# Optimization experiments

Hardware: AMD Instinct MI355X
Metric: run time of the kernel (lower is better)

The kernel has to match this reference:

```python
import jax, jax.numpy as jnp
import numpy as np

VOCAB = 32000
D = 256
NB = 32          # n_bubbles
NEQ = 5          # n_equilibrium_steps
SEQ = 64


def setup_inputs() -> dict:
    key = jax.random.key(0)
    k1, k2, k3 = jax.random.split(key, 3)
    tokens = jax.random.randint(k1, (SEQ,), 0, VOCAB)
    E = jax.random.normal(k2, (VOCAB, D), dtype=jnp.float32) * 0.02
    bubbles = jax.random.normal(k3, (NB, D), dtype=jnp.float32) * 0.02
    return {
        "tokens": tokens,
        "E": E,
        "bubbles": bubbles,
        "memory_decay_base": jnp.float32(0.8),
        "novelty_sensitivity": jnp.float32(1.0),
    }


def _foam(bubbles, x):
    """Foam equilibrium stand-in.
    bubbles: [NB, D] learned bubble states; x: [D] input.
    Returns (equilibrium [NB,D], rho [D,D], output_dist [NB]).
    rho is a trace-1 density matrix over normalized bubble states.
    """
    scale = 1.0 / np.sqrt(D)
    s = bubbles
    for _ in range(NEQ):  # fixed small count of equilibrium steps
        w = jax.nn.softmax(s @ x * scale)            # [NB]
        s = s + w[:, None] * (x[None, :] - s)        # relax toward input
    p = jax.nn.softmax(s @ x * scale)                # output_dist [NB]
    sn = s / (jnp.linalg.norm(s, axis=-1, keepdims=True) + 1e-10)
    rho = jnp.einsum('b,bi,bj->ij', p, sn, sn)       # [D, D], trace == 1
    return s, rho, p


def reference(tokens, E, bubbles, memory_decay_base, novelty_sensitivity):
    sens = jnp.abs(novelty_sensitivity)

    def step(memory, tok):
        x = E[tok]                                   # [D]
        mm = memory.mean(axis=0)                     # [D]
        mem_norm = jnp.linalg.norm(mm) + 1e-10
        x_norm = jnp.linalg.norm(x) + 1e-10
        novelty = jnp.where(mem_norm > 1e-8,
                            1.0 - jnp.dot(x, mm) / (x_norm * mem_norm),
                            jnp.float32(1.0))
        decay = jax.nn.sigmoid(memory_decay_base - sens * novelty)
        x_wm = x + decay * mm
        eq, rho, p = _foam(bubbles, x_wm)
        memory = decay * memory + (1.0 - decay) * eq
        # Born rule: logit_v = e_v^T rho e_v   -> [VOCAB]
        logits = ((E @ rho) * E).sum(axis=-1)
        return memory, logits

    mem0 = jnp.zeros((NB, D), jnp.float32)
    _, logits = jax.lax.scan(step, mem0, tokens)
    return logits  # [SEQ, VOCAB]
```

## Files before the change

kernel.cpp:

```cpp
#include <hip/hip_runtime.h>
#include <math.h>

#define VOCAB 32000
#define D 256
#define NB 32
#define NEQ 5
#define SEQ 64
#define NBASIS 96

#define WS_S     0
#define WS_COEF  (NBASIS*NBASIS)
#define WS_U     (WS_COEF + SEQ*NBASIS)
#define WS_VV    (WS_U + SEQ*NB)
#define WS_C     (WS_VV + SEQ*NB)
#define WS_WHL   (WS_C + SEQ)

typedef __attribute__((ext_vector_type(8))) short short8v;
typedef __attribute__((ext_vector_type(4))) float f32x4;

__global__ __launch_bounds__(256) void foam_grams(
    const int* __restrict__ tokens, const float* __restrict__ E,
    const float* __restrict__ bubbles, float* __restrict__ ws)
{
    const int idx = blockIdx.x * 256 + threadIdx.x;
    const int i = idx / NBASIS, j = idx % NBASIS;
    const float4* ra = (const float4*)((i < NB) ? (bubbles + i * D)
                                                : (E + (long)tokens[i - NB] * D));
    const float4* rb = (const float4*)((j < NB) ? (bubbles + j * D)
                                                : (E + (long)tokens[j - NB] * D));
    float a0 = 0.f, a1 = 0.f, a2 = 0.f, a3 = 0.f;
    #pragma unroll
    for (int k = 0; k < D / 4; k += 4) {
        float4 x, y;
        x = ra[k];     y = rb[k];
        a0 = fmaf(x.x, y.x, fmaf(x.y, y.y, fmaf(x.z, y.z, fmaf(x.w, y.w, a0))));
        x = ra[k + 1]; y = rb[k + 1];
        a1 = fmaf(x.x, y.x, fmaf(x.y, y.y, fmaf(x.z, y.z, fmaf(x.w, y.w, a1))));
        x = ra[k + 2]; y = rb[k + 2];
        a2 = fmaf(x.x, y.x, fmaf(x.y, y.y, fmaf(x.z, y.z, fmaf(x.w, y.w, a2))));
        x = ra[k + 3]; y = rb[k + 3];
        a3 = fmaf(x.x, y.x, fmaf(x.y, y.y, fmaf(x.z, y.z, fmaf(x.w, y.w, a3))));
    }
    ws[WS_S + i * NBASIS + j] = (a0 + a1) + (a2 + a3);
}

template <int CTRL>
__device__ __forceinline__ float dpp_add(float x) {
    int yi = __builtin_amdgcn_update_dpp(0, __float_as_int(x), CTRL, 0xF, 0xF, true);
    return x + __int_as_float(yi);
}
__device__ __forceinline__ float xor16_add(float x) {
    float a, b;
    asm("v_mov_b32 %0, %2\n\t"
        "v_mov_b32 %1, %2\n\t"
        "v_permlane16_swap_b32 %0, %1"
        : "=&v"(a), "=&v"(b) : "v"(x));
    return a + b;
}
__device__ __forceinline__ float xor32_add(float x) {
    float a, b;
    asm("v_mov_b32 %0, %2\n\t"
        "v_mov_b32 %1, %2\n\t"
        "v_permlane32_swap_b32 %0, %1"
        : "=&v"(a), "=&v"(b) : "v"(x));
    return a + b;
}
__device__ __forceinline__ float sum32h(float x) {
    x = dpp_add<0xB1>(x);
    x = dpp_add<0x4E>(x);
    x = dpp_add<0x124>(x);
    x = dpp_add<0x128>(x);
    return xor16_add(x);
}
__device__ __forceinline__ float sum64(float x) {
    return xor32_add(sum32h(x));
}
__device__ __forceinline__ float rdlane(float v, int lane) {
    return __int_as_float(__builtin_amdgcn_readlane(__float_as_int(v), lane));
}
__device__ __forceinline__ float fast_rcp(float x) {
    float r; asm("v_rcp_f32 %0, %1" : "=v"(r) : "v"(x)); return r;
}
__device__ __forceinline__ float fast_sqrt(float x) {
    float r; asm("v_sqrt_f32 %0, %1" : "=v"(r) : "v"(x)); return r;
}
__device__ __forceinline__ float fast_exp2(float x) {
    float r; asm("v_exp_f32 %0, %1" : "=v"(r) : "v"(x)); return r;
}
__device__ __forceinline__ void split1(float x, short& hi, short& lo) {
    unsigned xb = __builtin_bit_cast(unsigned, x);
    unsigned hb = xb & 0xFFFF0000u;
    float fl = x - __builtin_bit_cast(float, hb);
    hi = (short)(hb >> 16);
    lo = (short)(__builtin_bit_cast(unsigned, fl) >> 16);
}

__global__ __launch_bounds__(64) void foam_scan5(
    const float* __restrict__ p_mdb, const float* __restrict__ p_ns,
    float* __restrict__ ws)
{
    const int l = threadIdx.x;
    const int b = l & 31;

    __shared__ float S2[SEQ][NBASIS];

    const float* wsS = ws + WS_S;
    for (int e = l; e < SEQ * NBASIS / 4; e += 64)
        ((float4*)S2)[e] = ((const float4*)(wsS + NB * NBASIS))[e];

    float gbb_row[NB];
    {
        const float4* pa = (const float4*)(wsS + b * NBASIS);
        #pragma unroll
        for (int i = 0; i < 8; ++i) {
            float4 va = pa[i];
            gbb_row[4*i] = va.x; gbb_row[4*i+1] = va.y;
            gbb_row[4*i+2] = va.z; gbb_row[4*i+3] = va.w;
        }
    }
    const float diag = wsS[(NB + l) * NBASIS + NB + l];
    const float bn2  = wsS[b * NBASIS + b];

    const float LOG2E = 1.44269504088896f;
    const float mdb2  = p_mdb[0] * LOG2E;
    const float sens2 = fabsf(p_ns[0]) * LOG2E;
    const float sl2e  = 0.0625f * LOG2E;

    __syncthreads();

    float y = 0.f, mm2 = 0.f;
    float m1 = 0.f, m2 = 0.f;

    float* wsCOEF = ws + WS_COEF;
    float* wsUV   = ws + WS_U;
    float* wsC    = ws + WS_C;

    float gxcol = S2[0][b];
    float xcol1 = S2[0][l];
    float xcol2 = S2[0][32 + l];

    const int uvoff = (l >> 5) * (SEQ * NB);

    #pragma unroll 4
    for (int t = 0; t < SEQ; ++t) {
        const float xdm = sum64(fmaf(xcol2, m2, xcol1 * m1));
        const float px  = rdlane(diag, t);
        const float nov = (mm2 > 9.8e-17f)
                        ? (1.f - xdm * fast_rcp(fast_sqrt(px * mm2)))
                        : 1.f;
        const float decay = fast_rcp(1.f + fast_exp2(fmaf(sens2, nov, -mdb2)));
        const float omd = 1.f - decay;

        wsCOEF[t * NBASIS + l] = fmaf(decay, m1, (l == NB + t) ? 1.f : 0.f);
        if (l >= 32)
            wsCOEF[t * NBASIS + 32 + l] = fmaf(decay, m2, (l == t) ? 1.f : 0.f);

        const float q = px + 2.f * decay * xdm + decay * decay * mm2;
        const float c = fmaf(decay, y, gxcol);

        const int tn = (t + 1) & (SEQ - 1);
        const float gxn = S2[tn][b];
        const float xn1 = S2[tn][l];
        const float xn2 = S2[tn][32 + l];

        const float cq2 = (c - q) * sl2e;
        float alpha = 1.f, p = 0.f;
        #pragma unroll
        for (int k = 0; k <= NEQ; ++k) {
            const float ev = fast_exp2(alpha * cq2);
            const float sm = sum32h(ev);
            const float r  = fast_rcp(sm);
            if (k < NEQ) {
                const float ae = alpha * ev;
                alpha = fmaf(-ae, r, alpha);
            } else {
                p = ev * r;
            }
        }

        const float oma = 1.f - alpha;
        const float s2v = alpha * alpha * bn2 + 2.f * alpha * oma * c + oma * oma * q;
        const float g = p * fast_rcp(s2v + 1e-20f);
        const float uu  = g * alpha * alpha;
        const float vv2 = 2.f * g * alpha * oma;
        wsUV[uvoff + t * NB + b] = (l < NB) ? uu : vv2;

        float asg[NB];
        #pragma unroll
        for (int j = 0; j < NB; ++j) asg[j] = rdlane(alpha, j);
        float ga0 = 0.f, ga1 = 0.f, ga2 = 0.f, ga3 = 0.f;
        #pragma unroll
        for (int j = 0; j < NB; j += 4) {
            ga0 = fmaf(gbb_row[j],     asg[j],     ga0);
            ga1 = fmaf(gbb_row[j + 1], asg[j + 1], ga1);
            ga2 = fmaf(gbb_row[j + 2], asg[j + 2], ga2);
            ga3 = fmaf(gbb_row[j + 3], asg[j + 3], ga3);
        }
        const float ga = (ga0 + ga1) + (ga2 + ga3);

        const float r0 = sum32h(alpha);
        const float r1 = sum32h(alpha * c);
        const float r2 = sum32h(alpha * y);
        const float r3 = sum32h(alpha * ga);
        const float Cp = sum32h(g * oma * oma);
        if (l == 0) wsC[t] = Cp;

        const float msc = (32.f - r0) * (1.f / 32.f);
        const float k1 = decay * fmaf(omd, msc, 1.f);
        const float mmxwm = fmaf(decay, mm2, xdm);
        const float mmms = fmaf(msc, mmxwm, r2 * (1.f / 32.f));
        const float u1sq = r3 * (1.f / 1024.f);
        const float msms = fmaf(msc * msc, q, fmaf(2.f * msc, r1 * (1.f / 32.f), u1sq));
        mm2 = decay * decay * mm2 + 2.f * decay * omd * mmms + omd * omd * msms;

        y = fmaf(k1, y, omd * fmaf(msc, gxcol, ga * (1.f / 32.f)));

        const float inc1 = (l < NB) ? omd * alpha * (1.f / 32.f)
                                    : ((l == NB + t) ? omd * msc : 0.f);
        m1 = fmaf(k1, m1, inc1);
        m2 = fmaf(k1, m2, (t >= NB && l == t) ? omd * msc : 0.f);

        gxcol = gxn;
        xcol1 = xn1;
        xcol2 = xn2;
    }
}

__global__ __launch_bounds__(256) void foam_recon(
    const int* __restrict__ tokens, const float* __restrict__ E,
    const float* __restrict__ bubbles, float* __restrict__ ws)
{
    const int i = blockIdx.x;
    const int d = threadIdx.x;
    __shared__ float cf[NBASIS];
    __shared__ int stok[SEQ];

    float val;
    if (i < NB) {
        val = bubbles[i * D + d];
    } else {
        const int t = i - NB;
        if (d < NBASIS) cf[d] = ws[WS_COEF + t * NBASIS + d];
        if (d < SEQ) stok[d] = tokens[d];
        __syncthreads();
        float acc = 0.f;
        #pragma unroll 8
        for (int bb = 0; bb < NB; ++bb) acc = fmaf(cf[bb], bubbles[bb * D + d], acc);
        #pragma unroll 8
        for (int j = 0; j < SEQ; ++j) acc = fmaf(cf[32 + j], E[(long)stok[j] * D + d], acc);
        val = acc;
    }
    short hi, lo;
    split1(val, hi, lo);
    unsigned short* Whl = (unsigned short*)(ws + WS_WHL);
    Whl[i * D + d]               = (unsigned short)hi;
    Whl[NBASIS * D + i * D + d]  = (unsigned short)lo;
}

#define MROWS 32
#define AS 264
#define HS 100
#define US 36

__global__ __launch_bounds__(512, 2) void foam_mfma_logits(
    const float* __restrict__ E,
    const float* __restrict__ ws,
    float* __restrict__ out)
{
    __shared__ short Ah[MROWS * AS];
    __shared__ short Al[MROWS * AS];
    __shared__ float H[MROWS][HS];
    __shared__ float us[SEQ * US];
    __shared__ float vs[SEQ * US];
    __shared__ float Cs[SEQ];

    const int tid = threadIdx.x;
    const int w = tid >> 6;
    const int l = tid & 63;
    const int lm = l & 15;
    const int lq = l >> 4;

    const long vb = (long)blockIdx.x * MROWS;

    {
        const float* src = E + vb * D;
        const int base = tid * 16;
        const int row = base >> 8;
        const int col = base & 255;
        float4 v0 = *(const float4*)(src + base);
        float4 v1 = *(const float4*)(src + base + 4);
        float4 v2 = *(const float4*)(src + base + 8);
        float4 v3 = *(const float4*)(src + base + 12);
        float f[16] = {v0.x,v0.y,v0.z,v0.w, v1.x,v1.y,v1.z,v1.w,
                       v2.x,v2.y,v2.z,v2.w, v3.x,v3.y,v3.z,v3.w};
        short8v h0, h1, l0, l1;
        #pragma unroll
        for (int j = 0; j < 8; ++j) { short hi, lo; split1(f[j], hi, lo); h0[j] = hi; l0[j] = lo; }
        #pragma unroll
        for (int j = 0; j < 8; ++j) { short hi, lo; split1(f[8+j], hi, lo); h1[j] = hi; l1[j] = lo; }
        *(short8v*)&Ah[row * AS + col]     = h0;
        *(short8v*)&Ah[row * AS + col + 8] = h1;
        *(short8v*)&Al[row * AS + col]     = l0;
        *(short8v*)&Al[row * AS + col + 8] = l1;
    }

    for (int i = tid; i < SEQ * NB; i += 512) {
        int t = i >> 5, bb = i & 31;
        us[t * US + bb] = ws[WS_U + i];
        vs[t * US + bb] = ws[WS_VV + i];
    }
    if (tid < SEQ) Cs[tid] = ws[WS_C + tid];
    __syncthreads();

    if (w < 6) {
        const int n = w * 16 + lm;
        const short* bh = (const short*)(ws + WS_WHL) + n * D + lq * 8;
        const short* bl = bh + NBASIS * D;
        const short* ar = &Ah[lm * AS + lq * 8];
        const short* al = &Al[lm * AS + lq * 8];

        f32x4 acc0 = {0.f,0.f,0.f,0.f}, acc1 = {0.f,0.f,0.f,0.f};

        #pragma unroll
        for (int ks = 0; ks < 8; ++ks) {
            const short8v bhi = *(const short8v*)(bh + ks * 32);
            const short8v blo = *(const short8v*)(bl + ks * 32);

            short8v ahi = *(const short8v*)(ar + ks * 32);
            short8v alo = *(const short8v*)(al + ks * 32);
            acc0 = __builtin_amdgcn_mfma_f32_16x16x32_bf16(ahi, bhi, acc0, 0, 0, 0);
            acc0 = __builtin_amdgcn_mfma_f32_16x16x32_bf16(ahi, blo, acc0, 0, 0, 0);
            acc0 = __builtin_amdgcn_mfma_f32_16x16x32_bf16(alo, bhi, acc0, 0, 0, 0);

            ahi = *(const short8v*)(ar + 16 * AS + ks * 32);
            alo = *(const short8v*)(al + 16 * AS + ks * 32);
            acc1 = __builtin_amdgcn_mfma_f32_16x16x32_bf16(ahi, bhi, acc1, 0, 0, 0);
            acc1 = __builtin_amdgcn_mfma_f32_16x16x32_bf16(ahi, blo, acc1, 0, 0, 0);
            acc1 = __builtin_amdgcn_mfma_f32_16x16x32_bf16(alo, bhi, acc1, 0, 0, 0);
        }
        #pragma unroll
        for (int r = 0; r < 4; ++r) {
            H[lq * 4 + r][w * 16 + lm]      = acc0[r];
            H[16 + lq * 4 + r][w * 16 + lm] = acc1[r];
        }
    }
    __syncthreads();

    const int t0 = w * 8 + lq;
    const int t1 = t0 + 4;
    const float c0 = Cs[t0], c1 = Cs[t1];

    #pragma unroll
    for (int mt = 0; mt < 2; ++mt) {
        const int row = mt * 16 + lm;
        float G[NB];
        #pragma unroll
        for (int i = 0; i < 8; ++i)
            *(float4*)&G[4 * i] = *(const float4*)&H[row][4 * i];

        float a0 = 0.f, b0 = 0.f, a1 = 0.f, b1 = 0.f;
        #pragma unroll
        for (int i = 0; i < 8; ++i) {
            float g0 = G[4*i], g1 = G[4*i+1], g2c = G[4*i+2], g3 = G[4*i+3];
            float q0 = g0*g0, q1 = g1*g1, q2 = g2c*g2c, q3 = g3*g3;
            float4 u0 = *(const float4*)&us[t0 * US + 4 * i];
            float4 v0 = *(const float4*)&vs[t0 * US + 4 * i];
            float4 u1 = *(const float4*)&us[t1 * US + 4 * i];
            float4 v1 = *(const float4*)&vs[t1 * US + 4 * i];
            a0 = fmaf(u0.x, q0, fmaf(u0.y, q1, fmaf(u0.z, q2, fmaf(u0.w, q3, a0))));
            b0 = fmaf(v0.x, g0, fmaf(v0.y, g1, fmaf(v0.z, g2c, fmaf(v0.w, g3, b0))));
            a1 = fmaf(u1.x, q0, fmaf(u1.y, q1, fmaf(u1.z, q2, fmaf(u1.w, q3, a1))));
            b1 = fmaf(v1.x, g0, fmaf(v1.y, g1, fmaf(v1.z, g2c, fmaf(v1.w, g3, b1))));
        }
        const float h0 = H[row][32 + t0];
        const float h1 = H[row][32 + t1];
        out[(long)t0 * VOCAB + vb + row] = fmaf(h0, b0, fmaf(h0 * h0, c0, a0));
        out[(long)t1 * VOCAB + vb + row] = fmaf(h1, b1, fmaf(h1 * h1, c1, a1));
    }
}

extern "C" void kernel_launch(void* const* d_in, const int* in_sizes, int n_in,
                              void* d_out, int out_size, void* d_ws, size_t ws_size,
                              hipStream_t stream) {
    const int*   tokens  = (const int*)d_in[0];
    const float* E       = (const float*)d_in[1];
    const float* bubbles = (const float*)d_in[2];
    const float* mdb     = (const float*)d_in[3];
    const float* ns      = (const float*)d_in[4];
    float* out = (float*)d_out;
    float* ws  = (float*)d_ws;

    hipLaunchKernelGGL(foam_grams, dim3((NBASIS * NBASIS) / 256), dim3(256), 0, stream,
                       tokens, E, bubbles, ws);
    hipLaunchKernelGGL(foam_scan5, dim3(1), dim3(64), 0, stream, mdb, ns, ws);
    hipLaunchKernelGGL(foam_recon, dim3(NBASIS), dim3(256), 0, stream,
                       tokens, E, bubbles, ws);
    hipLaunchKernelGGL(foam_mfma_logits, dim3(VOCAB / MROWS), dim3(512), 0, stream,
                       E, ws, out);
}
```

Measured before the change: 108.2 us.

## Overlap serial scan with vocab projection onto raw basis, add epilogue

The Gram computation and the bf16 split of the raw basis rows (bubbles plus token embeddings) are merged into one prep kernel. A fused kernel then runs the serial 64-step scan in block 0 while the other blocks project E onto the raw 96-vector basis with MFMA and write an H matrix to workspace. A separate epilogue applies the scan coefficients afterwards, so the scan no longer has to finish before the large GEMM starts. In exchange it writes and re-reads a VOCAB×96 float intermediate and needs a larger workspace, falling back to the old path when the workspace is too small.

```diff
diff --git a/kernel.cpp b/kernel.cpp
--- a/kernel.cpp
+++ b/kernel.cpp
@@ -14,35 +14,10 @@
 #define WS_VV    (WS_U + SEQ*NB)
 #define WS_C     (WS_VV + SEQ*NB)
 #define WS_WHL   (WS_C + SEQ)
+#define WS_HF    (WS_WHL + NBASIS*D/2*2)
 
 typedef __attribute__((ext_vector_type(8))) short short8v;
 typedef __attribute__((ext_vector_type(4))) float f32x4;
-
-__global__ __launch_bounds__(256) void foam_grams(
-    const int* __restrict__ tokens, const float* __restrict__ E,
-    const float* __restrict__ bubbles, float* __restrict__ ws)
-{
-    const int idx = blockIdx.x * 256 + threadIdx.x;
-    const int i = idx / NBASIS, j = idx % NBASIS;
-    const float4* ra = (const float4*)((i < NB) ? (bubbles + i * D)
-                                                : (E + (long)tokens[i - NB] * D));
-    const float4* rb = (const float4*)((j < NB) ? (bubbles + j * D)
-                                                : (E + (long)tokens[j - NB] * D));
-    float a0 = 0.f, a1 = 0.f, a2 = 0.f, a3 = 0.f;
-    #pragma unroll
-    for (int k = 0; k < D / 4; k += 4) {
-        float4 x, y;
-        x = ra[k];     y = rb[k];
-        a0 = fmaf(x.x, y.x, fmaf(x.y, y.y, fmaf(x.z, y.z, fmaf(x.w, y.w, a0))));
-        x = ra[k + 1]; y = rb[k + 1];
-        a1 = fmaf(x.x, y.x, fmaf(x.y, y.y, fmaf(x.z, y.z, fmaf(x.w, y.w, a1))));
-        x = ra[k + 2]; y = rb[k + 2];
-        a2 = fmaf(x.x, y.x, fmaf(x.y, y.y, fmaf(x.z, y.z, fmaf(x.w, y.w, a2))));
-        x = ra[k + 3]; y = rb[k + 3];
-        a3 = fmaf(x.x, y.x, fmaf(x.y, y.y, fmaf(x.z, y.z, fmaf(x.w, y.w, a3))));
-    }
-    ws[WS_S + i * NBASIS + j] = (a0 + a1) + (a2 + a3);
-}
 
 template <int CTRL>
 __device__ __forceinline__ float dpp_add(float x) {
@@ -95,192 +70,196 @@
     lo = (short)(__builtin_bit_cast(unsigned, fl) >> 16);
 }
 
-__global__ __launch_bounds__(64) void foam_scan5(
+__global__ __launch_bounds__(256) void foam_prep(
+    const int* __restrict__ tokens, const float* __restrict__ E,
+    const float* __restrict__ bubbles, float* __restrict__ ws)
+{
+    const int bid = blockIdx.x;
+    const int d = threadIdx.x;
+
+    {
+        const float val = (bid < NB) ? bubbles[bid * D + d]
+                                     : E[(long)tokens[bid - NB] * D + d];
+        short hi, lo;
+        split1(val, hi, lo);
+        unsigned short* Uhl = (unsigned short*)(ws + WS_WHL);
+        Uhl[bid * D + d]              = (unsigned short)hi;
+        Uhl[NBASIS * D + bid * D + d] = (unsigned short)lo;
+    }
+
+    const int idx = bid * 256 + d;
+    if (idx < NBASIS * NBASIS) {
+        const int i = idx / NBASIS, j = idx % NBASIS;
+        const float4* ra = (const float4*)((i < NB) ? (bubbles + i * D)
+                                                    : (E + (long)tokens[i - NB] * D));
+        const float4* rb = (const float4*)((j < NB) ? (bubbles + j * D)
+                                                    : (E + (long)tokens[j - NB] * D));
+        float a0 = 0.f, a1 = 0.f, a2 = 0.f, a3 = 0.f;
+        #pragma unroll
+        for (int k = 0; k < D / 4; k += 4) {
+            float4 x, y;
+            x = ra[k];     y = rb[k];
+            a0 = fmaf(x.x, y.x, fmaf(x.y, y.y, fmaf(x.z, y.z, fmaf(x.w, y.w, a0))));
+            x = ra[k + 1]; y = rb[k + 1];
+            a1 = fmaf(x.x, y.x, fmaf(x.y, y.y, fmaf(x.z, y.z, fmaf(x.w, y.w, a1))));
+            x = ra[k + 2]; y = rb[k + 2];
+            a2 = fmaf(x.x, y.x, fmaf(x.y, y.y, fmaf(x.z, y.z, fmaf(x.w, y.w, a2))));
+            x = ra[k + 3]; y = rb[k + 3];
+            a3 = fmaf(x.x, y.x, fmaf(x.y, y.y, fmaf(x.z, y.z, fmaf(x.w, y.w, a3))));
+        }
+        ws[WS_S + i * NBASIS + j] = (a0 + a1) + (a2 + a3);
+    }
+}
+
+#define MROWS 32
+#define AS 264
+
+__global__ __launch_bounds__(512) void foam_fused(
+    const float* __restrict__ E,
     const float* __restrict__ p_mdb, const float* __restrict__ p_ns,
     float* __restrict__ ws)
 {
-    const int l = threadIdx.x;
-    const int b = l & 31;
-
-    __shared__ float S2[SEQ][NBASIS];
-
-    const float* wsS = ws + WS_S;
-    for (int e = l; e < SEQ * NBASIS / 4; e += 64)
-        ((float4*)S2)[e] = ((const float4*)(wsS + NB * NBASIS))[e];
-
-    float gbb_row[NB];
-    {
-        const float4* pa = (const float4*)(wsS + b * NBASIS);
-        #pragma unroll
-        for (int i = 0; i < 8; ++i) {
-            float4 va = pa[i];
-            gbb_row[4*i] = va.x; gbb_row[4*i+1] = va.y;
-            gbb_row[4*i+2] = va.z; gbb_row[4*i+3] = va.w;
-        }
-    }
-    const float diag = wsS[(NB + l) * NBASIS + NB + l];
-    const float bn2  = wsS[b * NBASIS + b];
-
-    const float LOG2E = 1.44269504088896f;
-    const float mdb2  = p_mdb[0] * LOG2E;
-    const float sens2 = fabsf(p_ns[0]) * LOG2E;
-    const float sl2e  = 0.0625f * LOG2E;
-
-    __syncthreads();
-
-    float y = 0.f, mm2 = 0.f;
-    float m1 = 0.f, m2 = 0.f;
-
-    float* wsCOEF = ws + WS_COEF;
-    float* wsUV   = ws + WS_U;
-    float* wsC    = ws + WS_C;
-
-    float gxcol = S2[0][b];
-    float xcol1 = S2[0][l];
-    float xcol2 = S2[0][32 + l];
-
-    const int uvoff = (l >> 5) * (SEQ * NB);
-
-    #pragma unroll 4
-    for (int t = 0; t < SEQ; ++t) {
-        const float xdm = sum64(fmaf(xcol2, m2, xcol1 * m1));
-        const float px  = rdlane(diag, t);
-        const float nov = (mm2 > 9.8e-17f)
-                        ? (1.f - xdm * fast_rcp(fast_sqrt(px * mm2)))
-                        : 1.f;
-        const float decay = fast_rcp(1.f + fast_exp2(fmaf(sens2, nov, -mdb2)));
-        const float omd = 1.f - decay;
-
-        wsCOEF[t * NBASIS + l] = fmaf(decay, m1, (l == NB + t) ? 1.f : 0.f);
-        if (l >= 32)
-            wsCOEF[t * NBASIS + 32 + l] = fmaf(decay, m2, (l == t) ? 1.f : 0.f);
-
-        const float q = px + 2.f * decay * xdm + decay * decay * mm2;
-        const float c = fmaf(decay, y, gxcol);
-
-        const int tn = (t + 1) & (SEQ - 1);
-        const float gxn = S2[tn][b];
-        const float xn1 = S2[tn][l];
-        const float xn2 = S2[tn][32 + l];
-
-        const float cq2 = (c - q) * sl2e;
-        float alpha = 1.f, p = 0.f;
-        #pragma unroll
-        for (int k = 0; k <= NEQ; ++k) {
-            const float ev = fast_exp2(alpha * cq2);
-            const float sm = sum32h(ev);
-            const float r  = fast_rcp(sm);
-            if (k < NEQ) {
-                const float ae = alpha * ev;
-                alpha = fmaf(-ae, r, alpha);
-            } else {
-                p = ev * r;
+    __shared__ __align__(16) char smem[MROWS * AS * 2 * 2];
+    const int tid = threadIdx.x;
+
+    if (blockIdx.x == 0) {
+        float (*S2)[NBASIS] = (float (*)[NBASIS])smem;
+        const int l = tid;
+        const int b = l & 31;
+        const float* wsS = ws + WS_S;
+
+        for (int e = l; e < SEQ * NBASIS / 4; e += 64)
+            ((float4*)S2)[e] = ((const float4*)(wsS + NB * NBASIS))[e];
+
+        float gbb_row[NB];
+        {
+            const float4* pa = (const float4*)(wsS + b * NBASIS);
+            #pragma unroll
+            for (int i = 0; i < 8; ++i) {
+                float4 va = pa[i];
+                gbb_row[4*i] = va.x; gbb_row[4*i+1] = va.y;
+                gbb_row[4*i+2] = va.z; gbb_row[4*i+3] = va.w;
             }
         }
-
-        const float oma = 1.f - alpha;
-        const float s2v = alpha * alpha * bn2 + 2.f * alpha * oma * c + oma * oma * q;
-        const float g = p * fast_rcp(s2v + 1e-20f);
-        const float uu  = g * alpha * alpha;
-        const float vv2 = 2.f * g * alpha * oma;
-        wsUV[uvoff + t * NB + b] = (l < NB) ? uu : vv2;
-
-        float asg[NB];
-        #pragma unroll
-        for (int j = 0; j < NB; ++j) asg[j] = rdlane(alpha, j);
-        float ga0 = 0.f, ga1 = 0.f, ga2 = 0.f, ga3 = 0.f;
-        #pragma unroll
-        for (int j = 0; j < NB; j += 4) {
-            ga0 = fmaf(gbb_row[j],     asg[j],     ga0);
-            ga1 = fmaf(gbb_row[j + 1], asg[j + 1], ga1);
-            ga2 = fmaf(gbb_row[j + 2], asg[j + 2], ga2);
-            ga3 = fmaf(gbb_row[j + 3], asg[j + 3], ga3);
-        }
-        const float ga = (ga0 + ga1) + (ga2 + ga3);
-
-        const float r0 = sum32h(alpha);
-        const float r1 = sum32h(alpha * c);
-        const float r2 = sum32h(alpha * y);
-        const float r3 = sum32h(alpha * ga);
-        const float Cp = sum32h(g * oma * oma);
-        if (l == 0) wsC[t] = Cp;
-
-        const float msc = (32.f - r0) * (1.f / 32.f);
-        const float k1 = decay * fmaf(omd, msc, 1.f);
-        const float mmxwm = fmaf(decay, mm2, xdm);
-        const float mmms = fmaf(msc, mmxwm, r2 * (1.f / 32.f));
-        const float u1sq = r3 * (1.f / 1024.f);
-        const float msms = fmaf(msc * msc, q, fmaf(2.f * msc, r1 * (1.f / 32.f), u1sq));
-        mm2 = decay * decay * mm2 + 2.f * decay * omd * mmms + omd * omd * msms;
-
-        y = fmaf(k1, y, omd * fmaf(msc, gxcol, ga * (1.f / 32.f)));
-
-        const float inc1 = (l < NB) ? omd * alpha * (1.f / 32.f)
-                                    : ((l == NB + t) ? omd * msc : 0.f);
-        m1 = fmaf(k1, m1, inc1);
-        m2 = fmaf(k1, m2, (t >= NB && l == t) ? omd * msc : 0.f);
-
-        gxcol = gxn;
-        xcol1 = xn1;
-        xcol2 = xn2;
-    }
-}
-
-__global__ __launch_bounds__(256) void foam_recon(
-    const int* __restrict__ tokens, const float* __restrict__ E,
-    const float* __restrict__ bubbles, float* __restrict__ ws)
-{
-    const int i = blockIdx.x;
-    const int d = threadIdx.x;
-    __shared__ float cf[NBASIS];
-    __shared__ int stok[SEQ];
-
-    float val;
-    if (i < NB) {
-        val = bubbles[i * D + d];
-    } else {
-        const int t = i - NB;
-        if (d < NBASIS) cf[d] = ws[WS_COEF + t * NBASIS + d];
-        if (d < SEQ) stok[d] = tokens[d];
+        const float diag = wsS[(NB + (l & 63)) * NBASIS + NB + (l & 63)];
+        const float bn2  = wsS[b * NBASIS + b];
+
+        const float LOG2E = 1.44269504088896f;
+        const float mdb2  = p_mdb[0] * LOG2E;
+        const float sens2 = fabsf(p_ns[0]) * LOG2E;
+        const float sl2e  = 0.0625f * LOG2E;
+
         __syncthreads();
-        float acc = 0.f;
-        #pragma unroll 8
-        for (int bb = 0; bb < NB; ++bb) acc = fmaf(cf[bb], bubbles[bb * D + d], acc);
-        #pragma unroll 8
-        for (int j = 0; j < SEQ; ++j) acc = fmaf(cf[32 + j], E[(long)stok[j] * D + d], acc);
-        val = acc;
-    }
-    short hi, lo;
-    split1(val, hi, lo);
-    unsigned short* Whl = (unsigned short*)(ws + WS_WHL);
-    Whl[i * D + d]               = (unsigned short)hi;
-    Whl[NBASIS * D + i * D + d]  = (unsigned short)lo;
-}
-
-#define MROWS 32
-#define AS 264
-#define HS 100
-#define US 36
-
-__global__ __launch_bounds__(512, 2) void foam_mfma_logits(
-    const float* __restrict__ E,
-    const float* __restrict__ ws,
-    float* __restrict__ out)
-{
-    __shared__ short Ah[MROWS * AS];
-    __shared__ short Al[MROWS * AS];
-    __shared__ float H[MROWS][HS];
-    __shared__ float us[SEQ * US];
-    __shared__ float vs[SEQ * US];
-    __shared__ float Cs[SEQ];
-
-    const int tid = threadIdx.x;
+        if (l >= 64) return;
+
+        float y = 0.f, mm2 = 0.f;
+        float m1 = 0.f, m2 = 0.f;
+
+        float* wsCOEF = ws + WS_COEF;
+        float* wsUV   = ws + WS_U;
+        float* wsC    = ws + WS_C;
+
+        float gxcol = S2[0][b];
+        float xcol1 = S2[0][l];
+        float xcol2 = S2[0][32 + l];
+
+        const int uvoff = (l >> 5) * (SEQ * NB);
+
+        #pragma unroll 4
+        for (int t = 0; t < SEQ; ++t) {
+            const float xdm = sum64(fmaf(xcol2, m2, xcol1 * m1));
+            const float px  = rdlane(diag, t);
+            const float nov = (mm2 > 9.8e-17f)
+                            ? (1.f - xdm * fast_rcp(fast_sqrt(px * mm2)))
+                            : 1.f;
+            const float decay = fast_rcp(1.f + fast_exp2(fmaf(sens2, nov, -mdb2)));
+            const float omd = 1.f - decay;
+
+            wsCOEF[t * NBASIS + l] = fmaf(decay, m1, (l == NB + t) ? 1.f : 0.f);
+            if (l >= 32)
+                wsCOEF[t * NBASIS + 32 + l] = fmaf(decay, m2, (l == t) ? 1.f : 0.f);
+
+            const float q = px + 2.f * decay * xdm + decay * decay * mm2;
+            const float c = fmaf(decay, y, gxcol);
+
+            const int tn = (t + 1) & (SEQ - 1);
+            const float gxn = S2[tn][b];
+            const float xn1 = S2[tn][l];
+            const float xn2 = S2[tn][32 + l];
+
+            const float cq2 = (c - q) * sl2e;
+            float alpha = 1.f, p = 0.f;
+            #pragma unroll
+            for (int k = 0; k <= NEQ; ++k) {
+                const float ev = fast_exp2(alpha * cq2);
+                const float sm = sum32h(ev);
+                const float r  = fast_rcp(sm);
+                if (k < NEQ) {
+                    const float ae = alpha * ev;
+                    alpha = fmaf(-ae, r, alpha);
+                } else {
+                    p = ev * r;
+                }
+            }
+
+            const float oma = 1.f - alpha;
+            const float s2v = alpha * alpha * bn2 + 2.f * alpha * oma * c + oma * oma * q;
+            const float g = p * fast_rcp(s2v + 1e-20f);
+            const float uu  = g * alpha * alpha;
+            const float vv2 = 2.f * g * alpha * oma;
+            wsUV[uvoff + t * NB + b] = (l < NB) ? uu : vv2;
+
+            float asg[NB];
+            #pragma unroll
+            for (int j = 0; j < NB; ++j) asg[j] = rdlane(alpha, j);
+            float ga0 = 0.f, ga1 = 0.f, ga2 = 0.f, ga3 = 0.f;
+            #pragma unroll
+            for (int j = 0; j < NB; j += 4) {
+                ga0 = fmaf(gbb_row[j],     asg[j],     ga0);
+                ga1 = fmaf(gbb_row[j + 1], asg[j + 1], ga1);
+                ga2 = fmaf(gbb_row[j + 2], asg[j + 2], ga2);
+                ga3 = fmaf(gbb_row[j + 3], asg[j + 3], ga3);
+            }
+            const float ga = (ga0 + ga1) + (ga2 + ga3);
+
+            const float r0 = sum32h(alpha);
+            const float r1 = sum32h(alpha * c);
+            const float r2 = sum32h(alpha * y);
+            const float r3 = sum32h(alpha * ga);
+            const float Cp = sum32h(g * oma * oma);
+            if (l == 0) wsC[t] = Cp;
+
+            const float msc = (32.f - r0) * (1.f / 32.f);
+            const float k1 = decay * fmaf(omd, msc, 1.f);
+            const float mmxwm = fmaf(decay, mm2, xdm);
+            const float mmms = fmaf(msc, mmxwm, r2 * (1.f / 32.f));
+            const float u1sq = r3 * (1.f / 1024.f);
+            const float msms = fmaf(msc * msc, q, fmaf(2.f * msc, r1 * (1.f / 32.f), u1sq));
+            mm2 = decay * decay * mm2 + 2.f * decay * omd * mmms + omd * omd * msms;
+
+            y = fmaf(k1, y, omd * fmaf(msc, gxcol, ga * (1.f / 32.f)));
+
+            const float inc1 = (l < NB) ? omd * alpha * (1.f / 32.f)
+                                        : ((l == NB + t) ? omd * msc : 0.f);
+            m1 = fmaf(k1, m1, inc1);
+            m2 = fmaf(k1, m2, (t >= NB && l == t) ? omd * msc : 0.f);
+
+            gxcol = gxn;
+            xcol1 = xn1;
+            xcol2 = xn2;
+        }
+        return;
+    }
+
+    short* Ah = (short*)smem;
+    short* Al = Ah + MROWS * AS;
+
     const int w = tid >> 6;
     const int l = tid & 63;
     const int lm = l & 15;
     const int lq = l >> 4;
 
-    const long vb = (long)blockIdx.x * MROWS;
+    const long vb = (long)(blockIdx.x - 1) * MROWS;
 
     {
         const float* src = E + vb * D;
@@ -303,6 +282,309 @@
         *(short8v*)&Al[row * AS + col]     = l0;
         *(short8v*)&Al[row * AS + col + 8] = l1;
     }
+    __syncthreads();
+
+    if (w >= 6) return;
+
+    const int n = w * 16 + lm;
+    const short* bh = (const short*)(ws + WS_WHL) + n * D + lq * 8;
+    const short* bl = bh + NBASIS * D;
+    const short* ar = &Ah[lm * AS + lq * 8];
+    const short* al = &Al[lm * AS + lq * 8];
+
+    f32x4 acc0 = {0.f,0.f,0.f,0.f}, acc1 = {0.f,0.f,0.f,0.f};
+
+    #pragma unroll
+    for (int ks = 0; ks < 8; ++ks) {
+        const short8v bhi = *(const short8v*)(bh + ks * 32);
+        const short8v blo = *(const short8v*)(bl + ks * 32);
+
+        short8v ahi = *(const short8v*)(ar + ks * 32);
+        short8v alo = *(const short8v*)(al + ks * 32);
+        acc0 = __builtin_amdgcn_mfma_f32_16x16x32_bf16(ahi, bhi, acc0, 0, 0, 0);
+        acc0 = __builtin_amdgcn_mfma_f32_16x16x32_bf16(ahi, blo, acc0, 0, 0, 0);
+        acc0 = __builtin_amdgcn_mfma_f32_16x16x32_bf16(alo, bhi, acc0, 0, 0, 0);
+
+        ahi = *(const short8v*)(ar + 16 * AS + ks * 32);
+        alo = *(const short8v*)(al + 16 * AS + ks * 32);
+        acc1 = __builtin_amdgcn_mfma_f32_16x16x32_bf16(ahi, bhi, acc1, 0, 0, 0);
+        acc1 = __builtin_amdgcn_mfma_f32_16x16x32_bf16(ahi, blo, acc1, 0, 0, 0);
+        acc1 = __builtin_amdgcn_mfma_f32_16x16x32_bf16(alo, bhi, acc1, 0, 0, 0);
+    }
+
+    float* Hf = ws + WS_HF;
+    #pragma unroll
+    for (int r = 0; r < 4; ++r) {
+        Hf[(vb + lq * 4 + r) * NBASIS + w * 16 + lm]      = acc0[r];
+        Hf[(vb + 16 + lq * 4 + r) * NBASIS + w * 16 + lm] = acc1[r];
+    }
+}
+
+__global__ __launch_bounds__(256) void foam_epilogue(
+    const float* __restrict__ ws, float* __restrict__ out)
+{
+    __shared__ __align__(16) float cf[SEQ][NBASIS];
+    __shared__ __align__(16) float us[SEQ][NB];
+    __shared__ __align__(16) float vs[SEQ][NB];
+    __shared__ float Cs[SEQ];
+
+    const int tid = threadIdx.x;
+    for (int i = tid; i < SEQ * NBASIS / 4; i += 256)
+        ((float4*)cf)[i] = ((const float4*)(ws + WS_COEF))[i];
+    for (int i = tid; i < SEQ * NB / 4; i += 256) {
+        ((float4*)us)[i] = ((const float4*)(ws + WS_U))[i];
+        ((float4*)vs)[i] = ((const float4*)(ws + WS_VV))[i];
+    }
+    if (tid < SEQ) Cs[tid] = ws[WS_C + tid];
+    __syncthreads();
+
+    const long v = (long)blockIdx.x * 256 + tid;
+    const float4* hrow = (const float4*)(ws + WS_HF + v * NBASIS);
+
+    float Hr[NBASIS];
+    #pragma unroll
+    for (int i = 0; i < NBASIS / 4; ++i)
+        *(float4*)&Hr[4 * i] = hrow[i];
+    float G2[NB];
+    #pragma unroll
+    for (int i = 0; i < NB; ++i) G2[i] = Hr[i] * Hr[i];
+
+    for (int t = 0; t < SEQ; ++t) {
+        float h0 = 0.f, h1 = 0.f, h2 = 0.f, h3 = 0.f;
+        #pragma unroll
+        for (int i = 0; i < NBASIS / 4; ++i) {
+            const float4 c4 = *(const float4*)&cf[t][4 * i];
+            h0 = fmaf(c4.x, Hr[4*i],   h0);
+            h1 = fmaf(c4.y, Hr[4*i+1], h1);
+            h2 = fmaf(c4.z, Hr[4*i+2], h2);
+            h3 = fmaf(c4.w, Hr[4*i+3], h3);
+        }
+        const float h = (h0 + h1) + (h2 + h3);
+
+        float a0 = 0.f, a1 = 0.f, b0 = 0.f, b1 = 0.f;
+        #pragma unroll
+        for (int i = 0; i < NB / 4; ++i) {
+            const float4 u4 = *(const float4*)&us[t][4 * i];
+            const float4 v4 = *(const float4*)&vs[t][4 * i];
+            a0 = fmaf(u4.x, G2[4*i],   a0);
+            b0 = fmaf(v4.x, Hr[4*i],   b0);
+            a1 = fmaf(u4.y, G2[4*i+1], a1);
+            b1 = fmaf(v4.y, Hr[4*i+1], b1);
+            a0 = fmaf(u4.z, G2[4*i+2], a0);
+            b0 = fmaf(v4.z, Hr[4*i+2], b0);
+            a1 = fmaf(u4.w, G2[4*i+3], a1);
+            b1 = fmaf(v4.w, Hr[4*i+3], b1);
+        }
+        out[(long)t * VOCAB + v] = fmaf(h, b0 + b1, fmaf(h * h, Cs[t], a0 + a1));
+    }
+}
+
+__global__ __launch_bounds__(64) void foam_scan5(
+    const float* __restrict__ p_mdb, const float* __restrict__ p_ns,
+    float* __restrict__ ws)
+{
+    const int l = threadIdx.x;
+    const int b = l & 31;
+
+    __shared__ float S2[SEQ][NBASIS];
+
+    const float* wsS = ws + WS_S;
+    for (int e = l; e < SEQ * NBASIS / 4; e += 64)
+        ((float4*)S2)[e] = ((const float4*)(wsS + NB * NBASIS))[e];
+
+    float gbb_row[NB];
+    {
+        const float4* pa = (const float4*)(wsS + b * NBASIS);
+        #pragma unroll
+        for (int i = 0; i < 8; ++i) {
+            float4 va = pa[i];
+            gbb_row[4*i] = va.x; gbb_row[4*i+1] = va.y;
+            gbb_row[4*i+2] = va.z; gbb_row[4*i+3] = va.w;
+        }
+    }
+    const float diag = wsS[(NB + l) * NBASIS + NB + l];
+    const float bn2  = wsS[b * NBASIS + b];
+
+    const float LOG2E = 1.44269504088896f;
+    const float mdb2  = p_mdb[0] * LOG2E;
+    const float sens2 = fabsf(p_ns[0]) * LOG2E;
+    const float sl2e  = 0.0625f * LOG2E;
+
+    __syncthreads();
+
+    float y = 0.f, mm2 = 0.f;
+    float m1 = 0.f, m2 = 0.f;
+
+    float* wsCOEF = ws + WS_COEF;
+    float* wsUV   = ws + WS_U;
+    float* wsC    = ws + WS_C;
+
+    float gxcol = S2[0][b];
+    float xcol1 = S2[0][l];
+    float xcol2 = S2[0][32 + l];
+
+    const int uvoff = (l >> 5) * (SEQ * NB);
+
+    #pragma unroll 4
+    for (int t = 0; t < SEQ; ++t) {
+        const float xdm = sum64(fmaf(xcol2, m2, xcol1 * m1));
+        const float px  = rdlane(diag, t);
+        const float nov = (mm2 > 9.8e-17f)
+                        ? (1.f - xdm * fast_rcp(fast_sqrt(px * mm2)))
+                        : 1.f;
+        const float decay = fast_rcp(1.f + fast_exp2(fmaf(sens2, nov, -mdb2)));
+        const float omd = 1.f - decay;
+
+        wsCOEF[t * NBASIS + l] = fmaf(decay, m1, (l == NB + t) ? 1.f : 0.f);
+        if (l >= 32)
+            wsCOEF[t * NBASIS + 32 + l] = fmaf(decay, m2, (l == t) ? 1.f : 0.f);
+
+        const float q = px + 2.f * decay * xdm + decay * decay * mm2;
+        const float c = fmaf(decay, y, gxcol);
+
+        const int tn = (t + 1) & (SEQ - 1);
+        const float gxn = S2[tn][b];
+        const float xn1 = S2[tn][l];
+        const float xn2 = S2[tn][32 + l];
+
+        const float cq2 = (c - q) * sl2e;
+        float alpha = 1.f, p = 0.f;
+        #pragma unroll
+        for (int k = 0; k <= NEQ; ++k) {
+            const float ev = fast_exp2(alpha * cq2);
+            const float sm = sum32h(ev);
+            const float r  = fast_rcp(sm);
+            if (k < NEQ) {
+                const float ae = alpha * ev;
+                alpha = fmaf(-ae, r, alpha);
+            } else {
+                p = ev * r;
+            }
+        }
+
+        const float oma = 1.f - alpha;
+        const float s2v = alpha * alpha * bn2 + 2.f * alpha * oma * c + oma * oma * q;
+        const float g = p * fast_rcp(s2v + 1e-20f);
+        const float uu  = g * alpha * alpha;
+        const float vv2 = 2.f * g * alpha * oma;
+        wsUV[uvoff + t * NB + b] = (l < NB) ? uu : vv2;
+
+        float asg[NB];
+        #pragma unroll
+        for (int j = 0; j < NB; ++j) asg[j] = rdlane(alpha, j);
+        float ga0 = 0.f, ga1 = 0.f, ga2 = 0.f, ga3 = 0.f;
+        #pragma unroll
+        for (int j = 0; j < NB; j += 4) {
+            ga0 = fmaf(gbb_row[j],     asg[j],     ga0);
+            ga1 = fmaf(gbb_row[j + 1], asg[j + 1], ga1);
+            ga2 = fmaf(gbb_row[j + 2], asg[j + 2], ga2);
+            ga3 = fmaf(gbb_row[j + 3], asg[j + 3], ga3);
+        }
+        const float ga = (ga0 + ga1) + (ga2 + ga3);
+
+        const float r0 = sum32h(alpha);
+        const float r1 = sum32h(alpha * c);
+        const float r2 = sum32h(alpha * y);
+        const float r3 = sum32h(alpha * ga);
+        const float Cp = sum32h(g * oma * oma);
+        if (l == 0) wsC[t] = Cp;
+
+        const float msc = (32.f - r0) * (1.f / 32.f);
+        const float k1 = decay * fmaf(omd, msc, 1.f);
+        const float mmxwm = fmaf(decay, mm2, xdm);
+        const float mmms = fmaf(msc, mmxwm, r2 * (1.f / 32.f));
+        const float u1sq = r3 * (1.f / 1024.f);
+        const float msms = fmaf(msc * msc, q, fmaf(2.f * msc, r1 * (1.f / 32.f), u1sq));
+        mm2 = decay * decay * mm2 + 2.f * decay * omd * mmms + omd * omd * msms;
+
+        y = fmaf(k1, y, omd * fmaf(msc, gxcol, ga * (1.f / 32.f)));
+
+        const float inc1 = (l < NB) ? omd * alpha * (1.f / 32.f)
+                                    : ((l == NB + t) ? omd * msc : 0.f);
+        m1 = fmaf(k1, m1, inc1);
+        m2 = fmaf(k1, m2, (t >= NB && l == t) ? omd * msc : 0.f);
+
+        gxcol = gxn;
+        xcol1 = xn1;
+        xcol2 = xn2;
+    }
+}
+
+__global__ __launch_bounds__(256) void foam_recon(
+    const int* __restrict__ tokens, const float* __restrict__ E,
+    const float* __restrict__ bubbles, float* __restrict__ ws)
+{
+    const int i = blockIdx.x;
+    const int d = threadIdx.x;
+    __shared__ float cfs[NBASIS];
+    __shared__ int stok[SEQ];
+
+    float val;
+    if (i < NB) {
+        val = bubbles[i * D + d];
+    } else {
+        const int t = i - NB;
+        if (d < NBASIS) cfs[d] = ws[WS_COEF + t * NBASIS + d];
+        if (d < SEQ) stok[d] = tokens[d];
+        __syncthreads();
+        float acc = 0.f;
+        #pragma unroll 8
+        for (int bb = 0; bb < NB; ++bb) acc = fmaf(cfs[bb], bubbles[bb * D + d], acc);
+        #pragma unroll 8
+        for (int j = 0; j < SEQ; ++j) acc = fmaf(cfs[32 + j], E[(long)stok[j] * D + d], acc);
+        val = acc;
+    }
+    short hi, lo;
+    split1(val, hi, lo);
+    unsigned short* Whl = (unsigned short*)(ws + WS_WHL);
+    Whl[i * D + d]               = (unsigned short)hi;
+    Whl[NBASIS * D + i * D + d]  = (unsigned short)lo;
+}
+
+#define HS 100
+#define US 36
+
+__global__ __launch_bounds__(512, 2) void foam_mfma_logits(
+    const float* __restrict__ E,
+    const float* __restrict__ ws,
+    float* __restrict__ out)
+{
+    __shared__ short Ah[MROWS * AS];
+    __shared__ short Al[MROWS * AS];
+    __shared__ float H[MROWS][HS];
+    __shared__ float us[SEQ * US];
+    __shared__ float vs[SEQ * US];
+    __shared__ float Cs[SEQ];
+
+    const int tid = threadIdx.x;
+    const int w = tid >> 6;
+    const int l = tid & 63;
+    const int lm = l & 15;
+    const int lq = l >> 4;
+
+    const long vb = (long)blockIdx.x * MROWS;
+
+    {
+        const float* src = E + vb * D;
+        const int base = tid * 16;
+        const int row = base >> 8;
+        const int col = base & 255;
+        float4 v0 = *(const float4*)(src + base);
+        float4 v1 = *(const float4*)(src + base + 4);
+        float4 v2 = *(const float4*)(src + base + 8);
+        float4 v3 = *(const float4*)(src + base + 12);
+        float f[16] = {v0.x,v0.y,v0.z,v0.w, v1.x,v1.y,v1.z,v1.w,
+                       v2.x,v2.y,v2.z,v2.w, v3.x,v3.y,v3.z,v3.w};
+        short8v h0, h1, l0, l1;
+        #pragma unroll
+        for (int j = 0; j < 8; ++j) { short hi, lo; split1(f[j], hi, lo); h0[j] = hi; l0[j] = lo; }
+        #pragma unroll
+        for (int j = 0; j < 8; ++j) { short hi, lo; split1(f[8+j], hi, lo); h1[j] = hi; l1[j] = lo; }
+        *(short8v*)&Ah[row * AS + col]     = h0;
+        *(short8v*)&Ah[row * AS + col + 8] = h1;
+        *(short8v*)&Al[row * AS + col]     = l0;
+        *(short8v*)&Al[row * AS + col + 8] = l1;
+    }
 
     for (int i = tid; i < SEQ * NB; i += 512) {
         int t = i >> 5, bb = i & 31;
@@ -390,11 +672,21 @@
     float* out = (float*)d_out;
     float* ws  = (float*)d_ws;
 
-    hipLaunchKernelGGL(foam_grams, dim3((NBASIS * NBASIS) / 256), dim3(256), 0, stream,
+    const size_t need = ((size_t)WS_HF + (size_t)VOCAB * NBASIS) * sizeof(float);
+
+    hipLaunchKernelGGL(foam_prep, dim3(NBASIS), dim3(256), 0, stream,
                        tokens, E, bubbles, ws);
-    hipLaunchKernelGGL(foam_scan5, dim3(1), dim3(64), 0, stream, mdb, ns, ws);
-    hipLaunchKernelGGL(foam_recon, dim3(NBASIS), dim3(256), 0, stream,
-                       tokens, E, bubbles, ws);
-    hipLaunchKernelGGL(foam_mfma_logits, dim3(VOCAB / MROWS), dim3(512), 0, stream,
-                       E, ws, out);
-}
+
+    if (ws_size >= need) {
+        hipLaunchKernelGGL(foam_fused, dim3(VOCAB / MROWS + 1), dim3(512), 0, stream,
+                           E, mdb, ns, ws);
+        hipLaunchKernelGGL(foam_epilogue, dim3(VOCAB / 256), dim3(256), 0, stream,
+                           ws, out);
+    } else {
+        hipLaunchKernelGGL(foam_scan5, dim3(1), dim3(64), 0, stream, mdb, ns, ws);
+        hipLaunchKernelGGL(foam_recon, dim3(NBASIS), dim3(256), 0, stream,
+                           tokens, E, bubbles, ws);
+        hipLaunchKernelGGL(foam_mfma_logits, dim3(VOCAB / MROWS), dim3(512), 0, stream,
+                           E, ws, out);
+    }
+}
```

Measured after the change: 147.0 us. 1.36x slower.
